# Kernel optimization log

Hardware: AMD Instinct MI355X
Metric: run time of the kernel (lower is better)

## Reference

```python
import jax, jax.numpy as jnp
import numpy as np

B, N, DIM, H, POS_DIM = 8, 1024, 512, 8, 50
D = DIM // H


def setup_inputs() -> dict:
    key = jax.random.key(0)
    ks = jax.random.split(key, 7)
    s = 0.02
    return {
        "x": jax.random.normal(ks[0], (B, N, DIM), jnp.float32),
        "pos": jax.random.normal(ks[1], (1, N, N, POS_DIM), jnp.float32),
        "W_kv": jax.random.normal(ks[2], (2 * DIM, DIM), jnp.float32) * s,
        "W_out": jax.random.normal(ks[3], (DIM, DIM), jnp.float32) * s,
        "b_out": jax.random.normal(ks[4], (DIM,), jnp.float32) * s,
        "w_pos": jax.random.normal(ks[5], (POS_DIM,), jnp.float32) * s,
        "b_pos": jax.random.normal(ks[6], (1,), jnp.float32) * s,
    }


def reference(x, pos, W_kv, W_out, b_out, w_pos, b_pos):
    b, n, dim = x.shape
    h, d = H, dim // H
    scale = dim ** -0.5
    # to_kv: Linear(dim, 2*dim, bias=False); layout 'b n (kv h d)'
    kv = x @ W_kv.T                                   # (b, n, 2*dim)
    k = kv[..., :dim].reshape(b, n, h, d).transpose(0, 2, 1, 3)   # (b,h,n,d)
    v = kv[..., dim:].reshape(b, n, h, d).transpose(0, 2, 1, 3)   # (b,h,n,d)
    dots = jnp.einsum('bhid,bhjd->bhij', k, k) * scale            # (b,h,n,n)
    # map_pos(dots[...,None] + pos[None]) == dots*sum(w) + pos@w + bias (Linear is linear)
    pos_bias = jnp.einsum('ijp,p->ij', pos[0, :n, :n, :], w_pos)  # (n,n)
    scores = dots * jnp.sum(w_pos) + pos_bias + b_pos[0]
    attn = jax.nn.softmax(scores, axis=-1)
    out = jnp.einsum('bhij,bhjd->bhid', attn, v)                  # (b,h,n,d)
    out = out.transpose(0, 2, 1, 3).reshape(b, n, dim)            # (b,n,dim)
    return out @ W_out.T + b_out
```

## Files before the change

### kernel.cpp

```cpp
#include <hip/hip_runtime.h>

#define B_ 8
#define N_ 1024
#define DIM_ 512
#define H_ 8
#define D_ 64
#define PD_ 50
#define PBROWS 256

typedef __attribute__((ext_vector_type(4))) float f32x4;
typedef __attribute__((ext_vector_type(8))) __bf16 bf16x8;

__device__ __forceinline__ unsigned short f2bf(float f) {
    unsigned int u = __float_as_uint(f);
    u += 0x7FFFu + ((u >> 16) & 1u);
    return (unsigned short)(u >> 16);
}

__global__ __launch_bounds__(256) void cast_all(const float* __restrict__ x,
                                                const float* __restrict__ wkv,
                                                const float* __restrict__ wout,
                                                unsigned short* __restrict__ xb,
                                                unsigned short* __restrict__ wkvb,
                                                unsigned short* __restrict__ woutb) {
    const int bid = blockIdx.x;
    const float* src;
    unsigned short* dst;
    int idx;
    if (bid < 4096)      { src = x;    dst = xb;    idx = bid; }
    else if (bid < 4608) { src = wkv;  dst = wkvb;  idx = bid - 4096; }
    else                 { src = wout; dst = woutb; idx = bid - 4608; }
    int i = idx * 256 + threadIdx.x;
    float4 v = reinterpret_cast<const float4*>(src)[i];
    ushort4 o;
    o.x = f2bf(v.x); o.y = f2bf(v.y); o.z = f2bf(v.z); o.w = f2bf(v.w);
    reinterpret_cast<ushort4*>(dst)[i] = o;
}

__global__ __launch_bounds__(256) void pos_bias_kernel(const float* __restrict__ pos,
                                                       const float* __restrict__ w_pos,
                                                       float* __restrict__ pb) {
    __shared__ float buf[PBROWS * PD_];
    const int t = threadIdx.x;
    const size_t base = (size_t)blockIdx.x * (PBROWS * PD_);
    const float4* src = reinterpret_cast<const float4*>(pos + base);
    float4* dst = reinterpret_cast<float4*>(buf);
#pragma unroll 4
    for (int i = t; i < PBROWS * PD_ / 4; i += 256)
        dst[i] = src[i];
    __syncthreads();
    float acc = 0.f;
    const float* row = buf + t * PD_;
#pragma unroll
    for (int p = 0; p < PD_; p++) acc += row[p] * w_pos[p];
    pb[(size_t)blockIdx.x * PBROWS + t] = acc;
}

__global__ __launch_bounds__(256) void kv_gemm(const unsigned short* __restrict__ xb,
                                               const unsigned short* __restrict__ wb,
                                               unsigned short* __restrict__ kb,
                                               unsigned short* __restrict__ vt) {
    __shared__ __align__(16) unsigned short As[128][72];
    __shared__ __align__(16) unsigned short Bs[64][72];
    const int m0 = blockIdx.x * 128;
    const int n0 = blockIdx.y * 64;
    const int t = threadIdx.x;
    const int w = t >> 6, l = t & 63;
    const int wr = (w >> 1) * 64, wc = (w & 1) * 32;
    const int lr = l & 15, lg = l >> 4;
    const int ar = t >> 1, ac = (t & 1) * 32;
    const int br = t >> 2, bc = (t & 3) * 16;

    f32x4 acc[4][2] = {};

    for (int k0 = 0; k0 < DIM_; k0 += 64) {
        __syncthreads();
#pragma unroll
        for (int u = 0; u < 4; u++)
            *reinterpret_cast<bf16x8*>(&As[ar][ac + u * 8]) =
                *reinterpret_cast<const bf16x8*>(&xb[(size_t)(m0 + ar) * DIM_ + k0 + ac + u * 8]);
#pragma unroll
        for (int u = 0; u < 2; u++)
            *reinterpret_cast<bf16x8*>(&Bs[br][bc + u * 8]) =
                *reinterpret_cast<const bf16x8*>(&wb[(size_t)(n0 + br) * DIM_ + k0 + bc + u * 8]);
        __syncthreads();
#pragma unroll
        for (int kh = 0; kh < 2; kh++) {
            bf16x8 b0 = *reinterpret_cast<const bf16x8*>(&Bs[wc + lr][kh * 32 + lg * 8]);
            bf16x8 b1 = *reinterpret_cast<const bf16x8*>(&Bs[wc + 16 + lr][kh * 32 + lg * 8]);
#pragma unroll
            for (int fm = 0; fm < 4; fm++) {
                bf16x8 a = *reinterpret_cast<const bf16x8*>(&As[wr + fm * 16 + lr][kh * 32 + lg * 8]);
                acc[fm][0] = __builtin_amdgcn_mfma_f32_16x16x32_bf16(a, b0, acc[fm][0], 0, 0, 0);
                acc[fm][1] = __builtin_amdgcn_mfma_f32_16x16x32_bf16(a, b1, acc[fm][1], 0, 0, 0);
            }
        }
    }

#pragma unroll
    for (int fm = 0; fm < 4; fm++)
#pragma unroll
        for (int fn = 0; fn < 2; fn++) {
            int gn = n0 + wc + fn * 16 + lr;
#pragma unroll
            for (int i = 0; i < 4; i++) {
                int gm = m0 + wr + fm * 16 + lg * 4 + i;
                unsigned short bv = f2bf(acc[fm][fn][i]);
                int b = gm >> 10, nseq = gm & 1023;
                if (gn < DIM_) {
                    int h = gn >> 6, d = gn & 63;
                    kb[(((size_t)(b * H_ + h) * N_) + nseq) * D_ + d] = bv;
                } else {
                    int c = gn - DIM_;
                    int h = c >> 6, d = c & 63;
                    vt[(((size_t)(b * H_ + h) * D_) + d) * N_ + nseq] = bv;
                }
            }
        }
}

__global__ __launch_bounds__(256) void attn_kernel(const unsigned short* __restrict__ kb,
                                                   const unsigned short* __restrict__ vt,
                                                   const float* __restrict__ pb,
                                                   const float* __restrict__ w_pos,
                                                   unsigned short* __restrict__ oh) {
    const int bh = blockIdx.x;
    const int qp = blockIdx.y;
    const int b = bh >> 3, h = bh & 7;
    __shared__ __align__(16) unsigned short Ks[64][72];
    __shared__ __align__(16) unsigned short Vs[64][72];
    __shared__ __align__(16) unsigned short Ps[4][16][72];
    const int t = threadIdx.x, w = t >> 6, l = t & 63, lr = l & 15, lg = l >> 4;

    float sw = 0.f;
    for (int p = 0; p < PD_; p++) sw += w_pos[p];
    const float alpha = sw * 0.044194173824159216f;

    const unsigned short* kh = kb + (size_t)bh * N_ * D_;
    const unsigned short* vh = vt + (size_t)bh * D_ * N_;
    const int q0 = qp * 128;
    const int sr = t >> 2, sk = (t & 3) * 8;

    *reinterpret_cast<bf16x8*>(&Ks[sr][sk]) =
        *reinterpret_cast<const bf16x8*>(&kh[(size_t)(q0 + sr) * D_ + sk]);
    *reinterpret_cast<bf16x8*>(&Ks[sr][sk + 32]) =
        *reinterpret_cast<const bf16x8*>(&kh[(size_t)(q0 + sr) * D_ + sk + 32]);
    *reinterpret_cast<bf16x8*>(&Vs[sr][sk]) =
        *reinterpret_cast<const bf16x8*>(&kh[(size_t)(q0 + 64 + sr) * D_ + sk]);
    *reinterpret_cast<bf16x8*>(&Vs[sr][sk + 32]) =
        *reinterpret_cast<const bf16x8*>(&kh[(size_t)(q0 + 64 + sr) * D_ + sk + 32]);
    __syncthreads();
    const bf16x8 aqA0 = *reinterpret_cast<const bf16x8*>(&Ks[w * 16 + lr][lg * 8]);
    const bf16x8 aqA1 = *reinterpret_cast<const bf16x8*>(&Ks[w * 16 + lr][32 + lg * 8]);
    const bf16x8 aqB0 = *reinterpret_cast<const bf16x8*>(&Vs[w * 16 + lr][lg * 8]);
    const bf16x8 aqB1 = *reinterpret_cast<const bf16x8*>(&Vs[w * 16 + lr][32 + lg * 8]);
    __syncthreads();

    *reinterpret_cast<bf16x8*>(&Ks[sr][sk]) =
        *reinterpret_cast<const bf16x8*>(&kh[(size_t)sr * D_ + sk]);
    *reinterpret_cast<bf16x8*>(&Ks[sr][sk + 32]) =
        *reinterpret_cast<const bf16x8*>(&kh[(size_t)sr * D_ + sk + 32]);
    *reinterpret_cast<bf16x8*>(&Vs[sr][sk]) =
        *reinterpret_cast<const bf16x8*>(&vh[(size_t)sr * N_ + sk]);
    *reinterpret_cast<bf16x8*>(&Vs[sr][sk + 32]) =
        *reinterpret_cast<const bf16x8*>(&vh[(size_t)sr * N_ + sk + 32]);
    __syncthreads();

    float lA[4] = {0.f, 0.f, 0.f, 0.f}, lB[4] = {0.f, 0.f, 0.f, 0.f};
    f32x4 accA[4] = {}, accB[4] = {};

    for (int jt = 0; jt < 16; jt++) {
        const int j0 = jt * 64;

        bf16x8 bk[4][2];
#pragma unroll
        for (int fn = 0; fn < 4; fn++) {
            bk[fn][0] = *reinterpret_cast<const bf16x8*>(&Ks[fn * 16 + lr][lg * 8]);
            bk[fn][1] = *reinterpret_cast<const bf16x8*>(&Ks[fn * 16 + lr][32 + lg * 8]);
        }

        bf16x8 rk0, rk1, rv0, rv1;
        if (jt < 15) {
            const int jn = j0 + 64;
            rk0 = *reinterpret_cast<const bf16x8*>(&kh[(size_t)(jn + sr) * D_ + sk]);
            rk1 = *reinterpret_cast<const bf16x8*>(&kh[(size_t)(jn + sr) * D_ + sk + 32]);
            rv0 = *reinterpret_cast<const bf16x8*>(&vh[(size_t)sr * N_ + jn + sk]);
            rv1 = *reinterpret_cast<const bf16x8*>(&vh[(size_t)sr * N_ + jn + sk + 32]);
        }

        f32x4 sA[4] = {}, sB[4] = {};
#pragma unroll
        for (int fn = 0; fn < 4; fn++) {
            sA[fn] = __builtin_amdgcn_mfma_f32_16x16x32_bf16(aqA0, bk[fn][0], sA[fn], 0, 0, 0);
            sA[fn] = __builtin_amdgcn_mfma_f32_16x16x32_bf16(aqA1, bk[fn][1], sA[fn], 0, 0, 0);
            sB[fn] = __builtin_amdgcn_mfma_f32_16x16x32_bf16(aqB0, bk[fn][0], sB[fn], 0, 0, 0);
            sB[fn] = __builtin_amdgcn_mfma_f32_16x16x32_bf16(aqB1, bk[fn][1], sB[fn], 0, 0, 0);
        }

        bf16x8 bv[4][2];
#pragma unroll
        for (int fd = 0; fd < 4; fd++) {
            bv[fd][0] = *reinterpret_cast<const bf16x8*>(&Vs[fd * 16 + lr][lg * 8]);
            bv[fd][1] = *reinterpret_cast<const bf16x8*>(&Vs[fd * 16 + lr][32 + lg * 8]);
        }

#pragma unroll
        for (int fn = 0; fn < 4; fn++) {
            int gj = j0 + fn * 16 + lr;
#pragma unroll
            for (int i = 0; i < 4; i++) {
                int gq = q0 + w * 16 + lg * 4 + i;
                float p = __expf(sA[fn][i] * alpha + pb[(size_t)gq * N_ + gj]);
                lA[i] += p;
                Ps[w][lg * 4 + i][fn * 16 + lr] = f2bf(p);
            }
        }
        asm volatile("" ::: "memory");
        {
            bf16x8 pa0 = *reinterpret_cast<const bf16x8*>(&Ps[w][lr][lg * 8]);
            bf16x8 pa1 = *reinterpret_cast<const bf16x8*>(&Ps[w][lr][32 + lg * 8]);
#pragma unroll
            for (int fd = 0; fd < 4; fd++) {
                accA[fd] = __builtin_amdgcn_mfma_f32_16x16x32_bf16(pa0, bv[fd][0], accA[fd], 0, 0, 0);
                accA[fd] = __builtin_amdgcn_mfma_f32_16x16x32_bf16(pa1, bv[fd][1], accA[fd], 0, 0, 0);
            }
        }
        asm volatile("" ::: "memory");

#pragma unroll
        for (int fn = 0; fn < 4; fn++) {
            int gj = j0 + fn * 16 + lr;
#pragma unroll
            for (int i = 0; i < 4; i++) {
                int gq = q0 + 64 + w * 16 + lg * 4 + i;
                float p = __expf(sB[fn][i] * alpha + pb[(size_t)gq * N_ + gj]);
                lB[i] += p;
                Ps[w][lg * 4 + i][fn * 16 + lr] = f2bf(p);
            }
        }
        asm volatile("" ::: "memory");
        {
            bf16x8 pa0 = *reinterpret_cast<const bf16x8*>(&Ps[w][lr][lg * 8]);
            bf16x8 pa1 = *reinterpret_cast<const bf16x8*>(&Ps[w][lr][32 + lg * 8]);
#pragma unroll
            for (int fd = 0; fd < 4; fd++) {
                accB[fd] = __builtin_amdgcn_mfma_f32_16x16x32_bf16(pa0, bv[fd][0], accB[fd], 0, 0, 0);
                accB[fd] = __builtin_amdgcn_mfma_f32_16x16x32_bf16(pa1, bv[fd][1], accB[fd], 0, 0, 0);
            }
        }

        __syncthreads();
        if (jt < 15) {
            *reinterpret_cast<bf16x8*>(&Ks[sr][sk]) = rk0;
            *reinterpret_cast<bf16x8*>(&Ks[sr][sk + 32]) = rk1;
            *reinterpret_cast<bf16x8*>(&Vs[sr][sk]) = rv0;
            *reinterpret_cast<bf16x8*>(&Vs[sr][sk + 32]) = rv1;
        }
        __syncthreads();
    }

#pragma unroll
    for (int msk = 1; msk < 16; msk <<= 1)
#pragma unroll
        for (int i = 0; i < 4; i++) {
            lA[i] += __shfl_xor(lA[i], msk);
            lB[i] += __shfl_xor(lB[i], msk);
        }

#pragma unroll
    for (int fd = 0; fd < 4; fd++) {
        int dcol = h * 64 + fd * 16 + lr;
#pragma unroll
        for (int i = 0; i < 4; i++) {
            int gqA = q0 + w * 16 + lg * 4 + i;
            oh[((size_t)(b * N_ + gqA)) * DIM_ + dcol] = f2bf(accA[fd][i] / lA[i]);
            int gqB = gqA + 64;
            oh[((size_t)(b * N_ + gqB)) * DIM_ + dcol] = f2bf(accB[fd][i] / lB[i]);
        }
    }
}

__global__ __launch_bounds__(256) void out_gemm(const unsigned short* __restrict__ ohb,
                                                const unsigned short* __restrict__ wob,
                                                const float* __restrict__ b_out,
                                                float* __restrict__ out) {
    __shared__ __align__(16) unsigned short As[128][72];
    __shared__ __align__(16) unsigned short Bs[64][72];
    const int m0 = blockIdx.x * 128;
    const int n0 = blockIdx.y * 64;
    const int t = threadIdx.x;
    const int w = t >> 6, l = t & 63;
    const int wr = (w >> 1) * 64, wc = (w & 1) * 32;
    const int lr = l & 15, lg = l >> 4;
    const int ar = t >> 1, ac = (t & 1) * 32;
    const int br = t >> 2, bc = (t & 3) * 16;

    f32x4 acc[4][2] = {};

    for (int k0 = 0; k0 < DIM_; k0 += 64) {
        __syncthreads();
#pragma unroll
        for (int u = 0; u < 4; u++)
            *reinterpret_cast<bf16x8*>(&As[ar][ac + u * 8]) =
                *reinterpret_cast<const bf16x8*>(&ohb[(size_t)(m0 + ar) * DIM_ + k0 + ac + u * 8]);
#pragma unroll
        for (int u = 0; u < 2; u++)
            *reinterpret_cast<bf16x8*>(&Bs[br][bc + u * 8]) =
                *reinterpret_cast<const bf16x8*>(&wob[(size_t)(n0 + br) * DIM_ + k0 + bc + u * 8]);
        __syncthreads();
#pragma unroll
        for (int kh = 0; kh < 2; kh++) {
            bf16x8 b0 = *reinterpret_cast<const bf16x8*>(&Bs[wc + lr][kh * 32 + lg * 8]);
            bf16x8 b1 = *reinterpret_cast<const bf16x8*>(&Bs[wc + 16 + lr][kh * 32 + lg * 8]);
#pragma unroll
            for (int fm = 0; fm < 4; fm++) {
                bf16x8 a = *reinterpret_cast<const bf16x8*>(&As[wr + fm * 16 + lr][kh * 32 + lg * 8]);
                acc[fm][0] = __builtin_amdgcn_mfma_f32_16x16x32_bf16(a, b0, acc[fm][0], 0, 0, 0);
                acc[fm][1] = __builtin_amdgcn_mfma_f32_16x16x32_bf16(a, b1, acc[fm][1], 0, 0, 0);
            }
        }
    }

#pragma unroll
    for (int fm = 0; fm < 4; fm++)
#pragma unroll
        for (int fn = 0; fn < 2; fn++) {
            int gn = n0 + wc + fn * 16 + lr;
            float bias = b_out[gn];
#pragma unroll
            for (int i = 0; i < 4; i++) {
                int gm = m0 + wr + fm * 16 + lg * 4 + i;
                out[(size_t)gm * DIM_ + gn] = acc[fm][fn][i] + bias;
            }
        }
}

extern "C" void kernel_launch(void* const* d_in, const int* in_sizes, int n_in,
                              void* d_out, int out_size, void* d_ws, size_t ws_size,
                              hipStream_t stream) {
    const float* x     = (const float*)d_in[0];
    const float* pos   = (const float*)d_in[1];
    const float* W_kv  = (const float*)d_in[2];
    const float* W_out = (const float*)d_in[3];
    const float* b_out = (const float*)d_in[4];
    const float* w_pos = (const float*)d_in[5];

    char* ws = (char*)d_ws;
    unsigned short* xb   = (unsigned short*)(ws);
    unsigned short* wkv  = (unsigned short*)(ws + 8388608);
    unsigned short* wout = (unsigned short*)(ws + 9437184);
    unsigned short* kb   = (unsigned short*)(ws + 9961472);
    unsigned short* vt   = (unsigned short*)(ws + 18350080);
    float*          pb   = (float*)(ws + 26738688);
    unsigned short* oh   = (unsigned short*)(ws + 30932992);
    float*          out  = (float*)d_out;

    cast_all<<<4864, 256, 0, stream>>>(x, W_kv, W_out, xb, wkv, wout);
    pos_bias_kernel<<<4096, 256, 0, stream>>>(pos, w_pos, pb);
    kv_gemm<<<dim3(64, 16), 256, 0, stream>>>(xb, wkv, kb, vt);
    attn_kernel<<<dim3(64, 8), 256, 0, stream>>>(kb, vt, pb, w_pos, oh);
    out_gemm<<<dim3(64, 8), 256, 0, stream>>>(oh, wout, b_out, out);
}
```

Before: 120.5 us.

## Fuse positional-bias reduction and KV GEMM into one interleaved launch

```diff
diff --git a/kernel.cpp b/kernel.cpp
--- a/kernel.cpp
+++ b/kernel.cpp
@@ -37,34 +37,43 @@
     reinterpret_cast<ushort4*>(dst)[i] = o;
 }
 
-__global__ __launch_bounds__(256) void pos_bias_kernel(const float* __restrict__ pos,
-                                                       const float* __restrict__ w_pos,
-                                                       float* __restrict__ pb) {
-    __shared__ float buf[PBROWS * PD_];
+__global__ __launch_bounds__(256) void fused_pos_kv(const float* __restrict__ pos,
+                                                    const float* __restrict__ w_pos,
+                                                    float* __restrict__ pb,
+                                                    const unsigned short* __restrict__ xb,
+                                                    const unsigned short* __restrict__ wb,
+                                                    unsigned short* __restrict__ kb,
+                                                    unsigned short* __restrict__ vt) {
+    __shared__ __align__(16) char smem[PBROWS * PD_ * 4];
+    const int bid = blockIdx.x;
     const int t = threadIdx.x;
-    const size_t base = (size_t)blockIdx.x * (PBROWS * PD_);
-    const float4* src = reinterpret_cast<const float4*>(pos + base);
-    float4* dst = reinterpret_cast<float4*>(buf);
+
+    if ((bid % 9) != 8) {
+        const int pbid = (bid / 9) * 8 + (bid % 9);
+        float* buf = reinterpret_cast<float*>(smem);
+        const size_t base = (size_t)pbid * (PBROWS * PD_ / 2);
+        const float4* src = reinterpret_cast<const float4*>(pos + (size_t)pbid * (128 * PD_));
+        float4* dst = reinterpret_cast<float4*>(buf);
 #pragma unroll 4
-    for (int i = t; i < PBROWS * PD_ / 4; i += 256)
-        dst[i] = src[i];
-    __syncthreads();
-    float acc = 0.f;
-    const float* row = buf + t * PD_;
-#pragma unroll
-    for (int p = 0; p < PD_; p++) acc += row[p] * w_pos[p];
-    pb[(size_t)blockIdx.x * PBROWS + t] = acc;
-}
-
-__global__ __launch_bounds__(256) void kv_gemm(const unsigned short* __restrict__ xb,
-                                               const unsigned short* __restrict__ wb,
-                                               unsigned short* __restrict__ kb,
-                                               unsigned short* __restrict__ vt) {
-    __shared__ __align__(16) unsigned short As[128][72];
-    __shared__ __align__(16) unsigned short Bs[64][72];
-    const int m0 = blockIdx.x * 128;
-    const int n0 = blockIdx.y * 64;
-    const int t = threadIdx.x;
+        for (int i = t; i < 128 * PD_ / 4; i += 256)
+            dst[i] = src[i];
+        __syncthreads();
+        if (t < 128) {
+            float acc = 0.f;
+            const float* row = buf + t * PD_;
+#pragma unroll
+            for (int p = 0; p < PD_; p++) acc += row[p] * w_pos[p];
+            pb[(size_t)pbid * 128 + t] = acc;
+        }
+        return;
+    }
+
+    const int kvid = bid / 9;
+    const int m0 = (kvid & 63) * 128;
+    const int n0 = (kvid >> 6) * 64;
+    unsigned short (*As)[72] = reinterpret_cast<unsigned short (*)[72]>(smem);
+    unsigned short (*Bs)[72] = reinterpret_cast<unsigned short (*)[72]>(smem + 128 * 72 * 2);
+
     const int w = t >> 6, l = t & 63;
     const int wr = (w >> 1) * 64, wc = (w & 1) * 32;
     const int lr = l & 15, lg = l >> 4;
@@ -356,8 +365,7 @@
     float*          out  = (float*)d_out;
 
     cast_all<<<4864, 256, 0, stream>>>(x, W_kv, W_out, xb, wkv, wout);
-    pos_bias_kernel<<<4096, 256, 0, stream>>>(pos, w_pos, pb);
-    kv_gemm<<<dim3(64, 16), 256, 0, stream>>>(xb, wkv, kb, vt);
+    fused_pos_kv<<<9216, 256, 0, stream>>>(pos, w_pos, pb, xb, wkv, kb, vt);
     attn_kernel<<<dim3(64, 8), 256, 0, stream>>>(kb, vt, pb, w_pos, oh);
     out_gemm<<<dim3(64, 8), 256, 0, stream>>>(oh, wout, b_out, out);
 }
```

New measurement: 135.0 us. 1.12x slower.
